# Kernel optimization log

Measured on AMD Instinct MI355X. Metric: run time of the kernel, lower is better.

The kernel has to match this reference:

```python
import jax, jax.numpy as jnp
import numpy as np

B, C, H, W = 16, 512, 32, 32
NUM_HEADS = 8
GROUPS = 32
EPS = 1e-5


def setup_inputs() -> dict:
    key = jax.random.key(0)
    ks = jax.random.split(key, 3)
    x = jax.random.normal(ks[0], (B, C, H, W), dtype=jnp.float32)
    # Conv2d 1x1 weights stored as (out, in); init ~ fan-in scaled normal
    qkv_w = jax.random.normal(ks[1], (3 * C, C), dtype=jnp.float32) * (C ** -0.5)
    proj_w = jax.random.normal(ks[2], (C, C), dtype=jnp.float32) * (C ** -0.5)
    return {
        "x": x,
        "norm_w": jnp.ones((C,), jnp.float32),
        "norm_b": jnp.zeros((C,), jnp.float32),
        "qkv_w": qkv_w,
        "qkv_b": jnp.zeros((3 * C,), jnp.float32),
        "proj_w": proj_w,
        "proj_b": jnp.zeros((C,), jnp.float32),
    }


def reference(x, norm_w, norm_b, qkv_w, qkv_b, proj_w, proj_b):
    b, c, hh, ww = x.shape
    nh = NUM_HEADS
    hd = c // nh
    n = hh * ww

    # GroupNorm(32, C)
    xg = x.reshape(b, GROUPS, c // GROUPS, hh, ww)
    mean = xg.mean(axis=(2, 3, 4), keepdims=True)
    var = ((xg - mean) ** 2).mean(axis=(2, 3, 4), keepdims=True)
    hn = ((xg - mean) * jax.lax.rsqrt(var + EPS)).reshape(b, c, hh, ww)
    hn = hn * norm_w[None, :, None, None] + norm_b[None, :, None, None]

    # 1x1 conv QKV projection
    qkv = jnp.einsum('bchw,oc->bohw', hn, qkv_w) + qkv_b[None, :, None, None]
    # (B,3C,H,W) -> (B,3,nh,hd,N) -> (3,B,nh,N,hd)
    qkv = qkv.reshape(b, 3, nh, hd, n).transpose(1, 0, 2, 4, 3)
    q, k, v = qkv[0], qkv[1], qkv[2]

    scale = hd ** -0.5
    attn = jax.nn.softmax(jnp.einsum('bhnd,bhmd->bhnm', q, k) * scale, axis=-1)
    o = jnp.einsum('bhnm,bhmd->bhnd', attn, v)  # (B,nh,N,hd)
    o = o.transpose(0, 1, 3, 2).reshape(b, c, hh, ww)

    out = jnp.einsum('bchw,oc->bohw', o, proj_w) + proj_b[None, :, None, None]
    return out + x
```

## Files before the change

kernel.cpp:

```cpp
#include <hip/hip_runtime.h>
#include <cstdint>
#include <math.h>


typedef __bf16 bf16;
typedef __attribute__((ext_vector_type(8))) __bf16 bf16x8;
typedef __attribute__((ext_vector_type(4))) float f32x4;
typedef __attribute__((ext_vector_type(4))) short s16x4;

union U8 { uint4 u4; bf16x8 v; bf16 h[8]; };
union U4 { ushort4 u; bf16 h[4]; };
union UB4 { ushort4 u; s16x4 s; bf16 h[4]; };
union F4 { float4 v; float f[4]; };

typedef __attribute__((address_space(1))) void* gp1;
typedef __attribute__((address_space(3))) void* lp3;

__device__ __forceinline__ void async16(const void* g, void* l) {
  __builtin_amdgcn_global_load_lds((gp1)g, (lp3)l, 16, 0, 0);
}

#define LOG2E 1.44269504f

__global__ __launch_bounds__(256) void cvt_w(const float* __restrict__ qw,
                                             const float* __restrict__ pw,
                                             bf16* __restrict__ qwb,
                                             bf16* __restrict__ pwb) {
  int i = blockIdx.x * 256 + threadIdx.x;
  F4 v; bf16* dst;
  if (i < 196608) { v.v = ((const float4*)qw)[i]; dst = qwb + (size_t)i * 4; }
  else { v.v = ((const float4*)pw)[i - 196608]; dst = pwb + (size_t)(i - 196608) * 4; }
  U4 o;
#pragma unroll
  for (int j = 0; j < 4; j++) o.h[j] = (bf16)v.f[j];
  *(ushort4*)dst = o.u;
}

__global__ __launch_bounds__(256) void gn_stats(const float* __restrict__ x,
                                                float2* __restrict__ stats) {
  int bg = blockIdx.x;
  const float* base = x + (size_t)bg * 16384;
  int t = threadIdx.x;
  float s = 0.f, ss = 0.f;
#pragma unroll
  for (int p = 0; p < 16; p++) {
    F4 u; u.v = *(const float4*)(base + (size_t)(p * 256 + t) * 4);
#pragma unroll
    for (int i = 0; i < 4; i++) { float v = u.f[i]; s += v; ss += v * v; }
  }
  for (int off = 1; off < 64; off <<= 1) { s += __shfl_xor(s, off); ss += __shfl_xor(ss, off); }
  __shared__ float red[8];
  int w = t >> 6;
  if ((t & 63) == 0) { red[w] = s; red[4 + w] = ss; }
  __syncthreads();
  if (t == 0) {
    float S = red[0] + red[1] + red[2] + red[3];
    float SS = red[4] + red[5] + red[6] + red[7];
    float mean = S * (1.f / 16384.f);
    float var = SS * (1.f / 16384.f) - mean * mean;
    stats[bg] = make_float2(mean, rsqrtf(var + 1e-5f));
  }
}

__global__ __launch_bounds__(256) void gn_apply(const float* __restrict__ x,
                                                const float* __restrict__ nwp,
                                                const float* __restrict__ nbp,
                                                const float2* __restrict__ stats,
                                                bf16* __restrict__ hnt) {
  int b = blockIdx.z, nt = blockIdx.y, ct = blockIdx.x;
  int t = threadIdx.x, w = t >> 6, l = t & 63;
  int wc = w & 1, wn = w >> 1;
  int cb = ct * 128 + wc * 64 + (l & 7) * 8;
  int n0 = nt * 64 + wn * 32 + (l >> 3) * 4;
  float2 ms = stats[b * 32 + (cb >> 4)];
  float wgt[8], bia[8];
#pragma unroll
  for (int i = 0; i < 8; i++) {
    float wi = nwp[cb + i] * ms.y;
    wgt[i] = wi;
    bia[i] = nbp[cb + i] - ms.x * wi;
  }
  F4 in[8];
  const float* xb = x + ((size_t)b * 512 + cb) * 1024 + n0;
#pragma unroll
  for (int i = 0; i < 8; i++) in[i].v = *(const float4*)(xb + (size_t)i * 1024);
  bf16* ob = hnt + ((size_t)b * 1024 + n0) * 512 + cb;
#pragma unroll
  for (int j = 0; j < 4; j++) {
    U8 o;
#pragma unroll
    for (int i = 0; i < 8; i++) o.h[i] = (bf16)(in[i].f[j] * wgt[i] + bia[i]);
    *(uint4*)(ob + (size_t)j * 512) = o.u4;
  }
}

__device__ __forceinline__ void gemm_compute32(const bf16* __restrict__ rA,
                                               const bf16* __restrict__ rB,
                                               int aoff, int boff,
                                               f32x4 (&acc)[4][4]) {
  bf16x8 af[4], bfr[4];
#pragma unroll
  for (int i = 0; i < 4; i++) {
    af[i] = *(const bf16x8*)(rA + aoff + i * 512);
    bfr[i] = *(const bf16x8*)(rB + boff + i * 512);
  }
#pragma unroll
  for (int i = 0; i < 4; i++)
#pragma unroll
    for (int j = 0; j < 4; j++)
      acc[i][j] = __builtin_amdgcn_mfma_f32_16x16x32_bf16(af[i], bfr[j], acc[i][j], 0, 0, 0);
}

__device__ __forceinline__ void gemm_bt_core(const bf16* ga0, const bf16* gb0,
                                             bf16* A0, bf16* B0,
                                             bf16* A1, bf16* B1,
                                             f32x4 (&acc)[4][4], int w, int l) {
  const bf16* ga = ga0 + (size_t)(w * 16 + (l >> 2)) * 512 + (l & 3) * 8;
  const bf16* gb = gb0 + (size_t)(w * 16 + (l >> 2)) * 512 + (l & 3) * 8;
  int wr = w >> 1, wc = w & 1;
  int aoff = (wr * 64 + (l & 15)) * 32 + (l >> 4) * 8;
  int boff = (wc * 64 + (l & 15)) * 32 + (l >> 4) * 8;
  int soff = w * 16 * 32;

  async16(ga, A0 + soff);
  async16(ga + 64 * 512, A0 + soff + 64 * 32);
  async16(gb, B0 + soff);
  async16(gb + 64 * 512, B0 + soff + 64 * 32);
  __syncthreads();

  for (int k0 = 0; k0 < 512; k0 += 64) {
    async16(ga + k0 + 32, A1 + soff);
    async16(ga + 64 * 512 + k0 + 32, A1 + soff + 64 * 32);
    async16(gb + k0 + 32, B1 + soff);
    async16(gb + 64 * 512 + k0 + 32, B1 + soff + 64 * 32);
    gemm_compute32(A0, B0, aoff, boff, acc);
    __syncthreads();
    if (k0 + 64 < 512) {
      async16(ga + k0 + 64, A0 + soff);
      async16(ga + 64 * 512 + k0 + 64, A0 + soff + 64 * 32);
      async16(gb + k0 + 64, B0 + soff);
      async16(gb + 64 * 512 + k0 + 64, B0 + soff + 64 * 32);
    }
    gemm_compute32(A1, B1, aoff, boff, acc);
    __syncthreads();
  }
}

__global__ __launch_bounds__(256, 3) void qkv_gemm(const bf16* __restrict__ hnt,
                                                   const bf16* __restrict__ qwb,
                                                   const float* __restrict__ qb,
                                                   bf16* __restrict__ qsw,
                                                   bf16* __restrict__ ksw,
                                                   bf16* __restrict__ vsw) {
  __shared__ bf16 A0[128 * 32], B0[128 * 32], A1[128 * 32], B1[128 * 32];
  int b = blockIdx.z, mt = blockIdx.y, ot = blockIdx.x;
  int m0 = mt * 128, o0 = ot * 128;
  int t = threadIdx.x, w = t >> 6, l = t & 63;
  f32x4 acc[4][4] = {};
  gemm_bt_core(hnt + ((size_t)b * 1024 + m0) * 512, qwb + (size_t)o0 * 512,
               A0, B0, A1, B1, acc, w, l);

  int wr = w >> 1, wc = w & 1, quad = l >> 4, li = l & 15;
#pragma unroll
  for (int i = 0; i < 4; i++) {
    int gnb = m0 + wr * 64 + i * 16;
    int blk = gnb >> 4;
#pragma unroll
    for (int j = 0; j < 4; j++) {
      int go = o0 + wc * 64 + j * 16 + li;
      float bias = qb[go];
      if (ot < 8) {
        int c = (ot < 4) ? go : (go - 512);
        int hh = c >> 6, d = c & 63;
        int ks = d >> 5, dq = (d >> 3) & 3, jj = d & 7;
        bf16* base = ((ot < 4) ? qsw : ksw) + ((size_t)(b * 8 + hh) << 16)
                     + (blk * 2 + ks) * 512 + dq * 8 + jj;
#pragma unroll
        for (int r = 0; r < 4; r++)
          base[(quad * 4 + r) * 32] = (bf16)(acc[i][j][r] + bias);
      } else {
        int c = go - 1024;
        int hh = c >> 6, d = c & 63;
        int df = d >> 4, lv = d & 15;
        bf16* base = vsw + ((size_t)(b * 8 + hh) << 16)
                     + (blk * 4 + df) * 256 + (lv * 4 + quad) * 4;
        U4 pk;
#pragma unroll
        for (int r = 0; r < 4; r++) pk.h[r] = (bf16)(acc[i][j][r] + bias);
        *(ushort4*)base = pk.u;
      }
    }
  }
}

__device__ __forceinline__ void attn_stage(const bf16* __restrict__ kp,
                                           const bf16* __restrict__ vp, int c,
                                           f32x4 (&stc)[2][2],
                                           f32x4 (&stn)[2][2],
                                           U8 (&ka)[2], U8 (&kc)[2],
                                           UB4 (&vaI)[2][4],
                                           UB4 (&vaO)[2][4],
                                           const bf16x8 (&qfr)[2][2],
                                           float (&mrun)[2], f32x4 (&lacc)[2],
                                           f32x4 (&of)[4][2], const f32x4& ZZ) {
  __builtin_amdgcn_s_setprio(1);
#pragma unroll
  for (int kf = 0; kf < 2; kf++) {
    stn[0][kf] = __builtin_amdgcn_mfma_f32_16x16x32_bf16(ka[kf].v, qfr[0][0], ZZ, 0, 0, 0);
    stn[1][kf] = __builtin_amdgcn_mfma_f32_16x16x32_bf16(ka[kf].v, qfr[1][0], ZZ, 0, 0, 0);
    stn[0][kf] = __builtin_amdgcn_mfma_f32_16x16x32_bf16(kc[kf].v, qfr[0][1], stn[0][kf], 0, 0, 0);
    stn[1][kf] = __builtin_amdgcn_mfma_f32_16x16x32_bf16(kc[kf].v, qfr[1][1], stn[1][kf], 0, 0, 0);
  }
  __builtin_amdgcn_s_setprio(0);
  int cn = ((c + 2) & 31) * 2048;
#pragma unroll
  for (int kf = 0; kf < 2; kf++) {
    ka[kf].u4 = *(const uint4*)(kp + cn + kf * 1024);
    kc[kf].u4 = *(const uint4*)(kp + cn + kf * 1024 + 512);
  }
  int cv = ((c + 1) & 31) * 2048;
#pragma unroll
  for (int kf = 0; kf < 2; kf++)
#pragma unroll
    for (int df = 0; df < 4; df++)
      vaO[kf][df].u = *(const ushort4*)(vp + cv + kf * 1024 + df * 256);
  UB4 pfr[2][2];
#pragma unroll
  for (int qf = 0; qf < 2; qf++) {
    float mt = fmaxf(fmaxf(fmaxf(stc[qf][0][0], stc[qf][0][1]),
                           fmaxf(stc[qf][0][2], stc[qf][0][3])),
                     fmaxf(fmaxf(stc[qf][1][0], stc[qf][1][1]),
                           fmaxf(stc[qf][1][2], stc[qf][1][3])));
    if (__ballot(mt > mrun[qf] + 8.f)) {
      mt = fmaxf(mt, __shfl_xor(mt, 16));
      mt = fmaxf(mt, __shfl_xor(mt, 32));
      float mnew = fmaxf(mrun[qf], mt);
      float alpha = __builtin_amdgcn_exp2f(mrun[qf] - mnew);
      mrun[qf] = mnew;
#pragma unroll
      for (int r = 0; r < 4; r++) lacc[qf][r] *= alpha;
#pragma unroll
      for (int df = 0; df < 4; df++)
#pragma unroll
        for (int r = 0; r < 4; r++) of[df][qf][r] *= alpha;
    }
    float m = mrun[qf];
#pragma unroll
    for (int kf = 0; kf < 2; kf++)
#pragma unroll
      for (int r = 0; r < 4; r++) {
        float e = __builtin_amdgcn_exp2f(stc[qf][kf][r] - m);
        lacc[qf][r] += e;
        pfr[qf][kf].h[r] = (bf16)e;
      }
  }
  __builtin_amdgcn_s_setprio(1);
#pragma unroll
  for (int kf = 0; kf < 2; kf++)
#pragma unroll
    for (int df = 0; df < 4; df++)
#pragma unroll
      for (int qf = 0; qf < 2; qf++)
        of[df][qf] = __builtin_amdgcn_mfma_f32_16x16x16bf16_1k(vaI[kf][df].s, pfr[qf][kf].s, of[df][qf], 0, 0, 0);
  __builtin_amdgcn_s_setprio(0);
}

__global__ __launch_bounds__(256, 3) void attn(const bf16* __restrict__ qsw,
                                               const bf16* __restrict__ ksw,
                                               const bf16* __restrict__ vsw,
                                               bf16* __restrict__ ont) {
  int bh = blockIdx.x;
  int b = bh >> 3, h = bh & 7;
  int qt = blockIdx.y;
  int t = threadIdx.x, w = t >> 6, l = t & 63;
  int quad = l >> 4, li = l & 15;
  int q0 = qt * 128 + w * 32;

  int laneK = (li * 4 + quad) * 8;
  int laneV = (li * 4 + quad) * 4;
  const bf16* qp = qsw + ((size_t)bh << 16) + laneK;
  const bf16* kp = ksw + ((size_t)bh << 16) + laneK;
  const bf16* vp = vsw + ((size_t)bh << 16) + laneV;

  const float QS = 0.125f * LOG2E;
  bf16x8 qfr[2][2];
#pragma unroll
  for (int qf = 0; qf < 2; qf++)
#pragma unroll
    for (int ks = 0; ks < 2; ks++) {
      U8 u;
      u.u4 = *(const uint4*)(qp + (((q0 >> 4) + qf) * 2 + ks) * 512);
#pragma unroll
      for (int i = 0; i < 8; i++) u.h[i] = (bf16)((float)u.h[i] * QS);
      qfr[qf][ks] = u.v;
    }

  float mrun[2] = {-INFINITY, -INFINITY};
  f32x4 lacc[2] = {};
  f32x4 of[4][2] = {};
  const f32x4 ZZ = {0.f, 0.f, 0.f, 0.f};

  U8 ka[2], kc[2];
  UB4 va0[2][4], va1[2][4];
#pragma unroll
  for (int kf = 0; kf < 2; kf++) {
    ka[kf].u4 = *(const uint4*)(kp + kf * 1024);
    kc[kf].u4 = *(const uint4*)(kp + kf * 1024 + 512);
  }
#pragma unroll
  for (int kf = 0; kf < 2; kf++)
#pragma unroll
    for (int df = 0; df < 4; df++)
      va0[kf][df].u = *(const ushort4*)(vp + kf * 1024 + df * 256);
  f32x4 st0[2][2], st1[2][2];
  __builtin_amdgcn_s_setprio(1);
#pragma unroll
  for (int kf = 0; kf < 2; kf++) {
    st0[0][kf] = __builtin_amdgcn_mfma_f32_16x16x32_bf16(ka[kf].v, qfr[0][0], ZZ, 0, 0, 0);
    st0[1][kf] = __builtin_amdgcn_mfma_f32_16x16x32_bf16(ka[kf].v, qfr[1][0], ZZ, 0, 0, 0);
    st0[0][kf] = __builtin_amdgcn_mfma_f32_16x16x32_bf16(kc[kf].v, qfr[0][1], st0[0][kf], 0, 0, 0);
    st0[1][kf] = __builtin_amdgcn_mfma_f32_16x16x32_bf16(kc[kf].v, qfr[1][1], st0[1][kf], 0, 0, 0);
  }
  __builtin_amdgcn_s_setprio(0);
#pragma unroll
  for (int kf = 0; kf < 2; kf++) {
    ka[kf].u4 = *(const uint4*)(kp + 2048 + kf * 1024);
    kc[kf].u4 = *(const uint4*)(kp + 2048 + kf * 1024 + 512);
  }

  for (int c = 0; c < 32; c += 2) {
    attn_stage(kp, vp, c,     st0, st1, ka, kc, va0, va1, qfr, mrun, lacc, of, ZZ);
    attn_stage(kp, vp, c + 1, st1, st0, ka, kc, va1, va0, qfr, mrun, lacc, of, ZZ);
  }

#pragma unroll
  for (int qf = 0; qf < 2; qf++) {
    float lsum = (lacc[qf][0] + lacc[qf][1]) + (lacc[qf][2] + lacc[qf][3]);
    lsum += __shfl_xor(lsum, 16);
    lsum += __shfl_xor(lsum, 32);
    float inv = 1.f / lsum;
    bf16* ob = ont + ((size_t)b * 1024 + q0 + qf * 16 + li) * 512 + h * 64 + quad * 4;
#pragma unroll
    for (int df = 0; df < 4; df++) {
      U4 pk;
#pragma unroll
      for (int r = 0; r < 4; r++) pk.h[r] = (bf16)(of[df][qf][r] * inv);
      *(ushort4*)(ob + df * 16) = pk.u;
    }
  }
}

__global__ __launch_bounds__(256, 3) void proj_gemm(const bf16* __restrict__ ont,
                                                    const bf16* __restrict__ pwb,
                                                    const float* __restrict__ pb,
                                                    const float* __restrict__ x,
                                                    float* __restrict__ out) {
  __shared__ bf16 A0[128 * 32], B0[128 * 32], A1[128 * 32], B1[128 * 32];
  int b = blockIdx.z, mt = blockIdx.y, ot = blockIdx.x;
  int m0 = mt * 128, o0 = ot * 128;
  int t = threadIdx.x, w = t >> 6, l = t & 63;
  f32x4 acc[4][4] = {};
  gemm_bt_core(ont + ((size_t)b * 1024 + m0) * 512, pwb + (size_t)o0 * 512,
               A0, B0, A1, B1, acc, w, l);

  int wr = w >> 1, wc = w & 1, quad = l >> 4, li = l & 15;
#pragma unroll
  for (int i = 0; i < 4; i++) {
    int gn = m0 + wr * 64 + i * 16 + quad * 4;
#pragma unroll
    for (int j = 0; j < 4; j++) {
      int go = o0 + wc * 64 + j * 16 + li;
      float bias = pb[go];
      F4 xres; xres.v = *(const float4*)(x + ((size_t)b * 512 + go) * 1024 + gn);
      F4 o;
#pragma unroll
      for (int r = 0; r < 4; r++) o.f[r] = acc[i][j][r] + bias + xres.f[r];
      *(float4*)(out + ((size_t)b * 512 + go) * 1024 + gn) = o.v;
    }
  }
}

extern "C" void kernel_launch(void* const* d_in, const int* in_sizes, int n_in,
                              void* d_out, int out_size, void* d_ws, size_t ws_size,
                              hipStream_t stream) {
  const float* x  = (const float*)d_in[0];
  const float* nw = (const float*)d_in[1];
  const float* nb = (const float*)d_in[2];
  const float* qw = (const float*)d_in[3];
  const float* qb = (const float*)d_in[4];
  const float* pw = (const float*)d_in[5];
  const float* pb = (const float*)d_in[6];
  float* out = (float*)d_out;

  char* ws = (char*)d_ws;
  float2* stats = (float2*)ws;
  bf16* qwb = (bf16*)(ws + (64u << 10));
  bf16* pwb = (bf16*)(ws + (2u << 20));
  bf16* hnt = (bf16*)(ws + (4u << 20));
  bf16* qsw = (bf16*)(ws + (20u << 20));
  bf16* ksw = (bf16*)(ws + (36u << 20));
  bf16* vsw = (bf16*)(ws + (52u << 20));
  bf16* ont = hnt;

  cvt_w<<<1024, 256, 0, stream>>>(qw, pw, qwb, pwb);
  gn_stats<<<512, 256, 0, stream>>>(x, stats);
  gn_apply<<<dim3(4, 16, 16), 256, 0, stream>>>(x, nw, nb, stats, hnt);
  qkv_gemm<<<dim3(12, 8, 16), 256, 0, stream>>>(hnt, qwb, qb, qsw, ksw, vsw);
  attn<<<dim3(128, 8, 1), 256, 0, stream>>>(qsw, ksw, vsw, ont);
  proj_gemm<<<dim3(4, 8, 16), 256, 0, stream>>>(ont, pwb, pb, x, out);
}
```

Measured before the change: 235.7 us.

## Fuse weight conversion, GroupNorm stats and apply into one LDS-staged kernel

Merges the weight-to-bf16 conversion, GroupNorm statistics and GroupNorm apply into a single kernel with one block per (batch, group). Each block stages its 64KB group slice of x in LDS, so x is read from global memory once instead of twice, and two kernel launches plus the stats round trip go away. The cost is 64KB of LDS per block, which limits occupancy, and each thread now writes 16 channels per token position as two 16-byte stores.

```diff
diff --git a/kernel.cpp b/kernel.cpp
--- a/kernel.cpp
+++ b/kernel.cpp
@@ -22,75 +22,68 @@
 
 #define LOG2E 1.44269504f
 
-__global__ __launch_bounds__(256) void cvt_w(const float* __restrict__ qw,
-                                             const float* __restrict__ pw,
-                                             bf16* __restrict__ qwb,
-                                             bf16* __restrict__ pwb) {
-  int i = blockIdx.x * 256 + threadIdx.x;
-  F4 v; bf16* dst;
-  if (i < 196608) { v.v = ((const float4*)qw)[i]; dst = qwb + (size_t)i * 4; }
-  else { v.v = ((const float4*)pw)[i - 196608]; dst = pwb + (size_t)(i - 196608) * 4; }
-  U4 o;
-#pragma unroll
-  for (int j = 0; j < 4; j++) o.h[j] = (bf16)v.f[j];
-  *(ushort4*)dst = o.u;
-}
-
-__global__ __launch_bounds__(256) void gn_stats(const float* __restrict__ x,
-                                                float2* __restrict__ stats) {
-  int bg = blockIdx.x;
-  const float* base = x + (size_t)bg * 16384;
+__global__ __launch_bounds__(256) void gn_fused(const float* __restrict__ x,
+                                                const float* __restrict__ nwp,
+                                                const float* __restrict__ nbp,
+                                                const float* __restrict__ qw,
+                                                const float* __restrict__ pw,
+                                                bf16* __restrict__ qwb,
+                                                bf16* __restrict__ pwb,
+                                                bf16* __restrict__ hnt) {
+  __shared__ float xs[16384];
+  __shared__ float red[8];
+  int bg = blockIdx.x, b = bg >> 5, g = bg & 31;
   int t = threadIdx.x;
+#pragma unroll
+  for (int k = 0; k < 2; k++) {
+    int i = bg * 512 + k * 256 + t;
+    F4 v; bf16* dst;
+    if (i < 196608) { v.v = ((const float4*)qw)[i]; dst = qwb + (size_t)i * 4; }
+    else { v.v = ((const float4*)pw)[i - 196608]; dst = pwb + (size_t)(i - 196608) * 4; }
+    U4 o;
+#pragma unroll
+    for (int j = 0; j < 4; j++) o.h[j] = (bf16)v.f[j];
+    *(ushort4*)dst = o.u;
+  }
+  const float* xb = x + (size_t)bg * 16384;
   float s = 0.f, ss = 0.f;
 #pragma unroll
-  for (int p = 0; p < 16; p++) {
-    F4 u; u.v = *(const float4*)(base + (size_t)(p * 256 + t) * 4);
+  for (int ci = 0; ci < 16; ci++) {
+    F4 u; u.v = *(const float4*)(xb + ci * 1024 + t * 4);
+    *(float4*)(xs + ci * 1024 + t * 4) = u.v;
 #pragma unroll
     for (int i = 0; i < 4; i++) { float v = u.f[i]; s += v; ss += v * v; }
   }
   for (int off = 1; off < 64; off <<= 1) { s += __shfl_xor(s, off); ss += __shfl_xor(ss, off); }
-  __shared__ float red[8];
   int w = t >> 6;
   if ((t & 63) == 0) { red[w] = s; red[4 + w] = ss; }
   __syncthreads();
-  if (t == 0) {
-    float S = red[0] + red[1] + red[2] + red[3];
-    float SS = red[4] + red[5] + red[6] + red[7];
-    float mean = S * (1.f / 16384.f);
-    float var = SS * (1.f / 16384.f) - mean * mean;
-    stats[bg] = make_float2(mean, rsqrtf(var + 1e-5f));
-  }
-}
-
-__global__ __launch_bounds__(256) void gn_apply(const float* __restrict__ x,
-                                                const float* __restrict__ nwp,
-                                                const float* __restrict__ nbp,
-                                                const float2* __restrict__ stats,
-                                                bf16* __restrict__ hnt) {
-  int b = blockIdx.z, nt = blockIdx.y, ct = blockIdx.x;
-  int t = threadIdx.x, w = t >> 6, l = t & 63;
-  int wc = w & 1, wn = w >> 1;
-  int cb = ct * 128 + wc * 64 + (l & 7) * 8;
-  int n0 = nt * 64 + wn * 32 + (l >> 3) * 4;
-  float2 ms = stats[b * 32 + (cb >> 4)];
-  float wgt[8], bia[8];
-#pragma unroll
-  for (int i = 0; i < 8; i++) {
-    float wi = nwp[cb + i] * ms.y;
+  float S = red[0] + red[1] + red[2] + red[3];
+  float SS = red[4] + red[5] + red[6] + red[7];
+  float mean = S * (1.f / 16384.f);
+  float rstd = rsqrtf(SS * (1.f / 16384.f) - mean * mean + 1e-5f);
+  int c0 = g * 16;
+  float wgt[16], bia[16];
+#pragma unroll
+  for (int i = 0; i < 16; i++) {
+    float wi = nwp[c0 + i] * rstd;
     wgt[i] = wi;
-    bia[i] = nbp[cb + i] - ms.x * wi;
-  }
-  F4 in[8];
-  const float* xb = x + ((size_t)b * 512 + cb) * 1024 + n0;
-#pragma unroll
-  for (int i = 0; i < 8; i++) in[i].v = *(const float4*)(xb + (size_t)i * 1024);
-  bf16* ob = hnt + ((size_t)b * 1024 + n0) * 512 + cb;
+    bia[i] = nbp[c0 + i] - mean * wi;
+  }
+  int n0 = t * 4;
+  F4 xv[16];
+#pragma unroll
+  for (int ci = 0; ci < 16; ci++) xv[ci].v = *(const float4*)(xs + ci * 1024 + n0);
+  bf16* ob = hnt + ((size_t)b * 1024 + n0) * 512 + c0;
 #pragma unroll
   for (int j = 0; j < 4; j++) {
-    U8 o;
-#pragma unroll
-    for (int i = 0; i < 8; i++) o.h[i] = (bf16)(in[i].f[j] * wgt[i] + bia[i]);
-    *(uint4*)(ob + (size_t)j * 512) = o.u4;
+    U8 o0, o1;
+#pragma unroll
+    for (int ci = 0; ci < 8; ci++) o0.h[ci] = (bf16)(xv[ci].f[j] * wgt[ci] + bia[ci]);
+#pragma unroll
+    for (int ci = 0; ci < 8; ci++) o1.h[ci] = (bf16)(xv[ci + 8].f[j] * wgt[ci + 8] + bia[ci + 8]);
+    *(uint4*)(ob + (size_t)j * 512) = o0.u4;
+    *(uint4*)(ob + (size_t)j * 512 + 8) = o1.u4;
   }
 }
 
@@ -393,7 +386,6 @@
   float* out = (float*)d_out;
 
   char* ws = (char*)d_ws;
-  float2* stats = (float2*)ws;
   bf16* qwb = (bf16*)(ws + (64u << 10));
   bf16* pwb = (bf16*)(ws + (2u << 20));
   bf16* hnt = (bf16*)(ws + (4u << 20));
@@ -402,9 +394,7 @@
   bf16* vsw = (bf16*)(ws + (52u << 20));
   bf16* ont = hnt;
 
-  cvt_w<<<1024, 256, 0, stream>>>(qw, pw, qwb, pwb);
-  gn_stats<<<512, 256, 0, stream>>>(x, stats);
-  gn_apply<<<dim3(4, 16, 16), 256, 0, stream>>>(x, nw, nb, stats, hnt);
+  gn_fused<<<512, 256, 0, stream>>>(x, nw, nb, qw, pw, qwb, pwb, hnt);
   qkv_gemm<<<dim3(12, 8, 16), 256, 0, stream>>>(hnt, qwb, qb, qsw, ksw, vsw);
   attn<<<dim3(128, 8, 1), 256, 0, stream>>>(qsw, ksw, vsw, ont);
   proj_gemm<<<dim3(4, 8, 16), 256, 0, stream>>>(ont, pwb, pb, x, out);
```

Result: faster. 230.9 us, median of 2 (-2.0%).
